# Kernel tuning notes

Measured on AMD Instinct MI355X. Metric: run time of the kernel, lower is better.

Reference implementation:

```python
import jax, jax.numpy as jnp
import numpy as np

EPS = 1e-5

def prelu(x, a):
    return jnp.where(x >= 0, x, a * x)

def batch_norm(x, axes):
    # training-mode BatchNorm with gamma=1, beta=0 (init values)
    m = jnp.mean(x, axis=axes, keepdims=True)
    v = jnp.var(x, axis=axes, keepdims=True)
    return (x - m) / jnp.sqrt(v + EPS)

def conv_branch(X, w, b):
    # X: [B,N,F]; Conv2d(1,1,(1,k)) over the feature axis, VALID
    lhs = X[:, None, :, :]                      # [B,1,N,F]
    rhs = w.reshape(1, 1, 1, -1)                # OIHW
    out = jax.lax.conv_general_dilated(lhs, rhs, (1, 1), 'VALID',
        dimension_numbers=('NCHW', 'OIHW', 'NCHW'))
    return out[:, 0] + b                        # [B,N,F-k+1]

def setup_inputs() -> dict:
    key = jax.random.key(0)
    ks = jax.random.split(key, 16)
    B, N, F, H, D = 8192, 29, 147, 4, 128
    d_cat = 429
    s = 0.05
    return {
        'X': jax.random.normal(ks[0], (B, N, F), jnp.float32),
        'corr': jax.random.uniform(ks[1], (B, N, N), jnp.float32),
        'w_c1': s * jax.random.normal(ks[2], (3,), jnp.float32),
        'b_c1': jnp.zeros((1,), jnp.float32),
        'w_c2': s * jax.random.normal(ks[3], (5,), jnp.float32),
        'b_c2': jnp.zeros((1,), jnp.float32),
        'w_c3': s * jax.random.normal(ks[4], (7,), jnp.float32),
        'b_c3': jnp.zeros((1,), jnp.float32),
        'a_cnn': 0.25 * jnp.ones((1,), jnp.float32),
        'Wg': s * jax.random.normal(ks[5], (d_cat, D), jnp.float32),
        'bg': jnp.zeros((D,), jnp.float32),
        'a_gnn': 0.25 * jnp.ones((1,), jnp.float32),
        'centroids': jax.random.normal(ks[6], (H, 1, D), jnp.float32),
        'head_w': s * jax.random.normal(ks[7], (H,), jnp.float32),
        'Wp': s * jax.random.normal(ks[8], (D, D), jnp.float32),
        'bp': jnp.zeros((D,), jnp.float32),
        'Wm1': s * jax.random.normal(ks[9], (D, D), jnp.float32),
        'bm1': jnp.zeros((D,), jnp.float32),
        'a_mlp': 0.25 * jnp.ones((1,), jnp.float32),
        'Wm2': s * jax.random.normal(ks[10], (D, 1), jnp.float32),
        'bm2': jnp.zeros((1,), jnp.float32),
    }

def reference(X, corr, w_c1, b_c1, w_c2, b_c2, w_c3, b_c3, a_cnn,
              Wg, bg, a_gnn, centroids, head_w, Wp, bp,
              Wm1, bm1, a_mlp, Wm2, bm2):
    # three conv branches + concat + PReLU + BN over node channels
    a1 = conv_branch(X, w_c1, b_c1)             # [B,29,145]
    a2 = conv_branch(X, w_c2, b_c2)             # [B,29,143]
    a3 = conv_branch(X, w_c3, b_c3)             # [B,29,141]
    x = prelu(jnp.concatenate([a1, a2, a3], axis=2), a_cnn)  # [B,29,429]
    x = batch_norm(x, (0, 2))
    # GraphConv: A x W + b
    x = jnp.einsum('bnm,bmd->bnd', corr, x) @ Wg + bg        # [B,29,128]
    x = prelu(x, a_gnn)
    x = batch_norm(x, (0, 2))
    # CoSimPool: multi-head cosine-sim attention assignment to 1 cluster
    xn = x / (jnp.linalg.norm(x, axis=-1, keepdims=True) + 1e-8)
    cn = centroids / (jnp.linalg.norm(centroids, axis=-1, keepdims=True) + 1e-8)
    sim = jnp.einsum('hmd,bnd->bhmn', cn, xn)                # [B,4,1,29]
    agg = jnp.einsum('h,bhmn->bmn', head_w, sim)             # 1x1 conv over heads
    C = jax.nn.softmax(agg, axis=-1)                         # [B,1,29]
    x = jnp.einsum('bmn,bnd->bmd', C, x) @ Wp + bp           # [B,1,128]
    x = x[:, 0]                                              # squeeze(1)
    x = batch_norm(x, (0,))
    h = prelu(x @ Wm1 + bm1, a_mlp)
    y = jax.nn.sigmoid(h @ Wm2 + bm2)                        # [B,1]
    return y
```

## Files before the change

### kernel.cpp

```cpp
#include <hip/hip_runtime.h>

#define B_    8192
#define N_    29
#define F_    147
#define DC    429
#define D_    128
#define ROWS  (B_*N_)
#define EPSBN 1e-5f

#define UTSTR   4096
#define RS_SH   3712

#define X3_OFF   16777216
#define ACC_OFF  (X3_OFF + B_*D_)
#define BN1_OFF  (ACC_OFF)
#define BN2_OFF  (ACC_OFF + 1856)
#define BN3_OFF  (ACC_OFF + 3712)
#define FIN_OFF  (ACC_OFF + 11904)
#define CSW_OFF  (FIN_OFF + 384)
#define V_OFF    (FIN_OFF + 512)
#define V1_OFF   (FIN_OFF + 640)
#define CSWP_OFF (FIN_OFF + 768)
#define IMG_OFF  (FIN_OFF + 1024)
#define WPI_OFF  (IMG_OFF + 28672)
#define WM1I_OFF (WPI_OFF + 8192)

typedef __bf16 bf16x8 __attribute__((ext_vector_type(8)));
typedef float  f32x4  __attribute__((ext_vector_type(4)));
typedef float  f32x2  __attribute__((ext_vector_type(2)));

__device__ __forceinline__ unsigned short f2bf(float f) {
  __bf16 h = (__bf16)f;
  return __builtin_bit_cast(unsigned short, h);
}
__device__ __forceinline__ float bf2f(unsigned u16) {
  return __uint_as_float(u16 << 16);
}
__device__ __forceinline__ unsigned packbf(f32x2 v) {
  return (unsigned)f2bf(v[0]) | ((unsigned)f2bf(v[1]) << 16);
}
__device__ __forceinline__ f32x2 pfma(f32x2 a, float s, f32x2 c) {
  return __builtin_elementwise_fma(a, (f32x2){s, s}, c);
}
__device__ __forceinline__ f32x2 prelu2(f32x2 v, float a) {
  f32x2 z = (f32x2){0.f, 0.f};
  return __builtin_elementwise_fma(__builtin_elementwise_min(v, z), (f32x2){a, a},
                                   __builtin_elementwise_max(v, z));
}
__device__ __forceinline__ void gload_lds4(const float* g, void* l) {
  __builtin_amdgcn_global_load_lds((const __attribute__((address_space(1))) void*)g,
                                   (__attribute__((address_space(3))) void*)l, 4, 0, 0);
}

#define TSTR 460
#define XROW 148
#define UTILS 34
#define ATSTR 136

__global__ void k0_setup(const float* __restrict__ Wg, const float* __restrict__ Wp,
                         const float* __restrict__ Wm1, const float* __restrict__ cent,
                         const float* __restrict__ hw, float* __restrict__ ws)
{
  const int tid = threadIdx.x;
  if (blockIdx.x < 16) {
    __shared__ float cs_l[8];
    const int kb = blockIdx.x * 8;
    if (tid < 8) cs_l[tid] = 0.f;
    __syncthreads();
    unsigned short* img = (unsigned short*)(ws + IMG_OFF);
    for (int i = tid; i < 8*448; i += 256) {
      int kk = i / 448, dk = i - kk*448;
      int k = kb + kk;
      int d;
      if      (dk < 145)  d = dk;
      else if (dk == 145) d = -1;
      else if (dk < 289)  d = dk - 1;
      else if (dk == 289) d = -1;
      else if (dk < 431)  d = dk - 2;
      else                d = -1;
      float v = (d >= 0) ? Wg[(size_t)d*D_ + k] : 0.f;
      img[(size_t)k*448 + dk] = f2bf(v);
      if (d >= 0) atomicAdd(&cs_l[kk], v);
    }
    __syncthreads();
    if (tid < 8) ws[CSW_OFF + kb + tid] = cs_l[tid];
  } else if (blockIdx.x == 16) {
    unsigned short* wpi = (unsigned short*)(ws + WPI_OFF);
    for (int i = tid; i < 16384; i += 256) {
      int k = i >> 7, c = i & 127;
      wpi[c*128 + k] = f2bf(Wp[k*128 + c]);
    }
    if (tid < 128) {
      float s = 0.f;
      for (int k = 0; k < 128; ++k) s += Wp[k*128 + tid];
      ws[CSWP_OFF + tid] = s;
    }
  } else if (blockIdx.x == 17) {
    unsigned short* wmi = (unsigned short*)(ws + WM1I_OFF);
    for (int i = tid; i < 16384; i += 256) {
      int k = i >> 7, c = i & 127;
      wmi[c*128 + k] = f2bf(Wm1[k*128 + c]);
    }
  } else {
    const int wv = tid >> 6, lane = tid & 63;
    if (wv == 0) {
      float vk0 = 0.f, vk1 = 0.f;
      for (int h = 0; h < 4; ++h) {
        float c0 = cent[h*D_ + lane];
        float c1 = cent[h*D_ + 64 + lane];
        float s = c0*c0 + c1*c1;
        #pragma unroll
        for (int off = 32; off >= 1; off >>= 1) s += __shfl_xor(s, off);
        float w = hw[h] / (sqrtf(s) + 1e-8f);
        vk0 = fmaf(c0, w, vk0);
        vk1 = fmaf(c1, w, vk1);
      }
      ws[V_OFF + lane]      = vk0;
      ws[V_OFF + 64 + lane] = vk1;
      float t = vk0 + vk1;
      #pragma unroll
      for (int off = 32; off >= 1; off >>= 1) t += __shfl_xor(t, off);
      if (lane == 0) ws[V1_OFF] = t;
    } else {
      for (int i = tid - 64; i < 11904; i += 192) ws[ACC_OFF + i] = 0.f;
    }
  }
}

__global__ __launch_bounds__(256, 5) void k1_conv_gemm(
    const float* __restrict__ X,
    const float* __restrict__ wc1, const float* __restrict__ bc1,
    const float* __restrict__ wc2, const float* __restrict__ bc2,
    const float* __restrict__ wc3, const float* __restrict__ bc3,
    const float* __restrict__ acnn, float* __restrict__ ws)
{
  __shared__ __align__(16) unsigned short t_s[32*TSTR];
  const int tid = threadIdx.x;
  const int b = blockIdx.x;
  const int wv = tid >> 6, lane = tid & 63;
  const int lrow = lane & 15, quad = lane >> 4;

  {
    const float* Xb = X + (size_t)b * (N_ * F_);
    unsigned* xd = (unsigned*)t_s;
    const int r0 = wv*8, r1 = (r0 + 8 < 29) ? r0 + 8 : 29;
    for (int r = r0; r < r1; ++r) {
      const float* src = Xb + r*147;
      unsigned* dst = xd + r*XROW;
      gload_lds4(src + lane, dst);
      gload_lds4(src + 64 + lane, dst + 64);
      if (lane < 19) gload_lds4(src + 128 + lane, dst + 128);
    }
    asm volatile("s_waitcnt vmcnt(0)" ::: "memory");
    __builtin_amdgcn_sched_barrier(0);
  }

  const float c10 = wc1[0], c11 = wc1[1], c12 = wc1[2], b1 = bc1[0];
  const float c20 = wc2[0], c21 = wc2[1], c22 = wc2[2], c23 = wc2[3], c24 = wc2[4], b2 = bc2[0];
  const float c30 = wc3[0], c31 = wc3[1], c32 = wc3[2], c33 = wc3[3], c34 = wc3[4],
              c35 = wc3[5], c36 = wc3[6], b3 = bc3[0];
  const float ap = acnn[0];

  const int nC = tid >> 3, qC = tid & 7;
  const bool act = (nC < 29);
  const int f0 = qC * 18;
  const int nld = act ? nC : 28;
  float xv[24];
  {
    const f32x2* xp = (const f32x2*)((const float*)t_s + nld*XROW + f0);
    #pragma unroll
    for (int j = 0; j < 12; ++j) {
      f32x2 t = xp[j];
      xv[2*j] = t[0]; xv[2*j+1] = t[1];
    }
  }
  __syncthreads();

  for (int i = tid; i < 3*448; i += 256) {
    int r = i / 448, c = i - r*448;
    t_s[(29 + r)*TSTR + c] = 0;
  }
  for (int i = tid; i < 29*19; i += 256) {
    int n = i / 19, j = i - n*19;
    int col = (j == 0) ? 145 : ((j == 1) ? 289 : (429 + j));
    t_s[n*TSTR + col] = 0;
  }

  {
    f32x2 s1v = (f32x2){0.f,0.f}, s2v = (f32x2){0.f,0.f};
    float s1t = 0.f, s2t = 0.f;
    unsigned short* tr = t_s + nC*TSTR + f0;
    if (act) {
      const int np2 = (qC < 7) ? 9 : 8;
      const int np3 = (qC < 7) ? 9 : 7;
      #pragma unroll
      for (int j = 0; j < 9; ++j) {
        const int k = 2*j;
        f32x2 xA = (f32x2){xv[k],   xv[k+1]};
        f32x2 xB = (f32x2){xv[k+1], xv[k+2]};
        f32x2 xC = (f32x2){xv[k+2], xv[k+3]};
        {
          f32x2 v1 = pfma(xA,c10, pfma(xB,c11, pfma(xC,c12, (f32x2){b1,b1})));
          v1 = prelu2(v1, ap);
          s1v += v1; s2v = __builtin_elementwise_fma(v1, v1, s2v);
          *(unsigned*)(tr + k) = packbf(v1);
        }
        if (j < np2) {
          f32x2 xD = (f32x2){xv[k+3], xv[k+4]};
          f32x2 xE = (f32x2){xv[k+4], xv[k+5]};
          f32x2 v2 = pfma(xA,c20, pfma(xB,c21, pfma(xC,c22, pfma(xD,c23, pfma(xE,c24, (f32x2){b2,b2})))));
          v2 = prelu2(v2, ap);
          s1v += v2; s2v = __builtin_elementwise_fma(v2, v2, s2v);
          *(unsigned*)(tr + 146 + k) = packbf(v2);
        }
        if (j < np3) {
          f32x2 xD = (f32x2){xv[k+3], xv[k+4]};
          f32x2 xE = (f32x2){xv[k+4], xv[k+5]};
          f32x2 xF = (f32x2){xv[k+5], xv[k+6]};
          f32x2 xG = (f32x2){xv[k+6], xv[k+7]};
          f32x2 v3 = pfma(xA,c30, pfma(xB,c31, pfma(xC,c32, pfma(xD,c33, pfma(xE,c34, pfma(xF,c35, pfma(xG,c36, (f32x2){b3,b3})))))));
          v3 = prelu2(v3, ap);
          s1v += v3; s2v = __builtin_elementwise_fma(v3, v3, s2v);
          *(unsigned*)(tr + 290 + k) = packbf(v3);
        }
      }
      if (qC == 7) {
        float u1 = fmaf(xv[18],c10, fmaf(xv[19],c11, fmaf(xv[20],c12, b1)));
        u1 = (u1 >= 0.f) ? u1 : ap*u1;
        s1t += u1; s2t = fmaf(u1, u1, s2t);
        tr[18] = f2bf(u1);
        float u2 = fmaf(xv[16],c20, fmaf(xv[17],c21, fmaf(xv[18],c22, fmaf(xv[19],c23, fmaf(xv[20],c24, b2)))));
        u2 = (u2 >= 0.f) ? u2 : ap*u2;
        s1t += u2; s2t = fmaf(u2, u2, s2t);
        tr[146 + 16] = f2bf(u2);
        float u3 = fmaf(xv[14],c30, fmaf(xv[15],c31, fmaf(xv[16],c32, fmaf(xv[17],c33, fmaf(xv[18],c34, fmaf(xv[19],c35, fmaf(xv[20],c36, b3)))))));
        u3 = (u3 >= 0.f) ? u3 : ap*u3;
        s1t += u3; s2t = fmaf(u3, u3, s2t);
        tr[290 + 14] = f2bf(u3);
      }
    }
    float s1 = s1v[0] + s1v[1] + s1t;
    float s2 = s2v[0] + s2v[1] + s2t;
    #pragma unroll
    for (int off = 4; off >= 1; off >>= 1) {
      s1 += __shfl_xor(s1, off);
      s2 += __shfl_xor(s2, off);
    }
    if (act && qC == 0) {
      float* bn1 = ws + BN1_OFF + (size_t)(blockIdx.x & 31) * 58;
      atomicAdd(&bn1[nC*2+0], s1);
      atomicAdd(&bn1[nC*2+1], s2);
    }
  }
  __syncthreads();

  const int n0 = wv * 32;
  const unsigned short* imgp = (const unsigned short*)(ws + IMG_OFF);
  const unsigned short* gB0 = imgp + (size_t)(n0 + lrow)*448 + quad*8;
  const unsigned short* gB1 = gB0 + 16*448;
  const unsigned short* tA = t_s + quad*8;

  f32x4 a00 = (f32x4){0.f,0.f,0.f,0.f}, a01 = a00, a10 = a00, a11 = a00;
  bf16x8 Br0[4], Br1[4];
  #pragma unroll
  for (int j = 0; j < 4; ++j) {
    Br0[j] = *(const bf16x8*)(gB0 + j*32);
    Br1[j] = *(const bf16x8*)(gB1 + j*32);
  }
  #pragma unroll
  for (int ks = 0; ks < 14; ++ks) {
    bf16x8 Bc0 = Br0[ks & 3], Bc1 = Br1[ks & 3];
    if (ks < 10) {
      Br0[ks & 3] = *(const bf16x8*)(gB0 + (ks+4)*32);
      Br1[ks & 3] = *(const bf16x8*)(gB1 + (ks+4)*32);
    }
    bf16x8 A0 = *(const bf16x8*)(tA + lrow*TSTR + ks*32);
    bf16x8 A1 = *(const bf16x8*)(tA + (16+lrow)*TSTR + ks*32);
    a00 = __builtin_amdgcn_mfma_f32_16x16x32_bf16(A0, Bc0, a00, 0, 0, 0);
    a01 = __builtin_amdgcn_mfma_f32_16x16x32_bf16(A0, Bc1, a01, 0, 0, 0);
    a10 = __builtin_amdgcn_mfma_f32_16x16x32_bf16(A1, Bc0, a10, 0, 0, 0);
    a11 = __builtin_amdgcn_mfma_f32_16x16x32_bf16(A1, Bc1, a11, 0, 0, 0);
  }
  __syncthreads();

  {
    unsigned* ut32 = (unsigned*)t_s;
    const int fb0 = n0 + lrow, fb1 = n0 + 16 + lrow;
    #pragma unroll
    for (int jp = 0; jp < 2; ++jp) {
      int w = quad*2 + jp;
      ut32[fb0*17 + w]     = packbf((f32x2){a00[2*jp], a00[2*jp+1]});
      ut32[fb1*17 + w]     = packbf((f32x2){a01[2*jp], a01[2*jp+1]});
      ut32[fb0*17 + 8 + w] = packbf((f32x2){a10[2*jp], a10[2*jp+1]});
      ut32[fb1*17 + 8 + w] = packbf((f32x2){a11[2*jp], a11[2*jp+1]});
    }
  }
  __syncthreads();
  {
    const unsigned* u32t = (const unsigned*)t_s;
    unsigned short* ws16 = (unsigned short*)ws;
    unsigned* Ug = (unsigned*)(ws16 + (size_t)b * UTSTR);
    #pragma unroll
    for (int it = 0; it < 8; ++it) {
      int idx = tid + it*256;
      int f = idx >> 4, pr = idx & 15;
      Ug[f*16 + pr] = u32t[f*17 + pr];
    }
  }
}

__global__ void k2_bn1f(float* __restrict__ ws)
{
  const int n = threadIdx.x;
  if (n < 29) {
    float s1 = 0.f, s2 = 0.f;
    #pragma unroll 4
    for (int s = 0; s < 32; ++s) {
      s1 += ws[BN1_OFF + s*58 + n*2 + 0];
      s2 += ws[BN1_OFF + s*58 + n*2 + 1];
    }
    const float inv = 1.f / (float)(B_ * DC);
    float mean = s1 * inv;
    float var  = s2 * inv - mean * mean;
    ws[FIN_OFF + n]      = mean;
    ws[FIN_OFF + 32 + n] = rsqrtf(var + EPSBN);
  }
}

__global__ __launch_bounds__(256) void k3_gnn(
    const float* __restrict__ corr, const float* __restrict__ bg,
    const float* __restrict__ agnn, float* __restrict__ ws)
{
  __shared__ float cwf[841];
  __shared__ unsigned short a_s[32*40];
  __shared__ float m1s[29], is1s[29], cms[32];
  __shared__ float sts0[4][32], sts1[4][32], sts2[4][32];

  const int b = blockIdx.x, tid = threadIdx.x;
  const int wv = tid >> 6, lane = tid & 63;
  const int lrow = lane & 15, quad = lane >> 4;
  unsigned short* Utb = (unsigned short*)ws + (size_t)b * UTSTR;

  const int f0 = wv * 32;
  bf16x8 B0 = *(const bf16x8*)&Utb[(f0      + lrow)*32 + quad*8];
  bf16x8 B1 = *(const bf16x8*)&Utb[(f0 + 16 + lrow)*32 + quad*8];

  if (tid < 29) {
    m1s[tid]  = ws[FIN_OFF + tid];
    is1s[tid] = ws[FIN_OFF + 32 + tid];
  }
  const float* cb = corr + (size_t)b * 841;
  for (int i = tid; i < 841; i += 256) cwf[i] = cb[i];
  __syncthreads();

  {
    float pp[4];
    #pragma unroll
    for (int it = 0; it < 4; ++it) {
      int i = tid + it*256;
      int n = i >> 5, m = i & 31;
      bool val = (n < 29 && m < 29);
      float v = val ? cwf[n*29 + m] * is1s[m] : 0.f;
      a_s[n*40 + m] = f2bf(v);
      pp[it] = val ? v * m1s[m] : 0.f;
    }
    #pragma unroll
    for (int off = 16; off >= 1; off >>= 1) {
      #pragma unroll
      for (int it = 0; it < 4; ++it) pp[it] += __shfl_xor(pp[it], off);
    }
    #pragma unroll
    for (int it = 0; it < 4; ++it) {
      int i = tid + it*256;
      if ((i & 31) == 0 && (i >> 5) < 29) cms[i >> 5] = pp[it];
    }
  }
  __syncthreads();

  bf16x8 A0 = *(const bf16x8*)&a_s[lrow*40 + quad*8];
  bf16x8 A1 = *(const bf16x8*)&a_s[(16 + lrow)*40 + quad*8];
  f32x4 acc[2][2];
  acc[0][0] = (f32x4){0.f,0.f,0.f,0.f}; acc[0][1] = (f32x4){0.f,0.f,0.f,0.f};
  acc[1][0] = (f32x4){0.f,0.f,0.f,0.f}; acc[1][1] = (f32x4){0.f,0.f,0.f,0.f};
  acc[0][0] = __builtin_amdgcn_mfma_f32_16x16x32_bf16(A0, B0, acc[0][0], 0, 0, 0);
  acc[0][1] = __builtin_amdgcn_mfma_f32_16x16x32_bf16(A0, B1, acc[0][1], 0, 0, 0);
  acc[1][0] = __builtin_amdgcn_mfma_f32_16x16x32_bf16(A1, B0, acc[1][0], 0, 0, 0);
  acc[1][1] = __builtin_amdgcn_mfma_f32_16x16x32_bf16(A1, B1, acc[1][1], 0, 0, 0);
  __syncthreads();

  const float ag = agnn[0];
  const float vA  = ws[V_OFF  + f0 + lrow],      vB  = ws[V_OFF  + f0 + 16 + lrow];
  const float csA = ws[CSW_OFF + f0 + lrow],     csB = ws[CSW_OFF + f0 + 16 + lrow];
  const float bgA = bg[f0 + lrow],               bgB = bg[f0 + 16 + lrow];

  float psy[8], psy2[8], psv[8];
  #pragma unroll
  for (int mt = 0; mt < 2; ++mt) {
    #pragma unroll
    for (int i = 0; i < 4; ++i) {
      int idx = mt*4 + i;
      int n = mt*16 + quad*4 + i;
      float y0 = acc[mt][0][i] - cms[n & 31]*csA + bgA;
      float y1 = acc[mt][1][i] - cms[n & 31]*csB + bgB;
      y0 = (y0 >= 0.f) ? y0 : ag*y0;
      y1 = (y1 >= 0.f) ? y1 : ag*y1;
      if (n < 29) {
        Utb[n*D_ + f0 + lrow]      = f2bf(y0);
        Utb[n*D_ + f0 + 16 + lrow] = f2bf(y1);
      }
      psy[idx]  = y0 + y1;
      psy2[idx] = fmaf(y0, y0, y1*y1);
      psv[idx]  = fmaf(y0, vA, y1*vB);
    }
  }
  #pragma unroll
  for (int off = 8; off >= 1; off >>= 1) {
    #pragma unroll
    for (int idx = 0; idx < 8; ++idx) {
      psy[idx]  += __shfl_xor(psy[idx],  off);
      psy2[idx] += __shfl_xor(psy2[idx], off);
      psv[idx]  += __shfl_xor(psv[idx],  off);
    }
  }
  if (lrow == 0) {
    #pragma unroll
    for (int mt = 0; mt < 2; ++mt) {
      #pragma unroll
      for (int i = 0; i < 4; ++i) {
        int idx = mt*4 + i;
        int n = mt*16 + quad*4 + i;
        if (n < 29) {
          sts0[wv][n] = psy[idx];
          sts1[wv][n] = psy2[idx];
          sts2[wv][n] = psv[idx];
        }
      }
    }
  }
  __syncthreads();
  if (tid < 29) {
    float S1 = sts0[0][tid] + sts0[1][tid] + sts0[2][tid] + sts0[3][tid];
    float S2 = sts1[0][tid] + sts1[1][tid] + sts1[2][tid] + sts1[3][tid];
    float Sv = sts2[0][tid] + sts2[1][tid] + sts2[2][tid] + sts2[3][tid];
    float* rs = (float*)(Utb + RS_SH);
    rs[tid]      = S1;
    rs[29 + tid] = S2;
    rs[58 + tid] = Sv;
    float* bn2 = ws + BN2_OFF + (size_t)(b & 31) * 58;
    atomicAdd(&bn2[tid*2+0], S1);
    atomicAdd(&bn2[tid*2+1], S2);
  }
}

__global__ __launch_bounds__(256) void k4_pool(
    const float* __restrict__ bpv, float* __restrict__ ws)
{
  __shared__ unsigned short Atile[32*ATSTR];
  __shared__ float m2s[29], is2s[29], koffs[32];
  const int tid = threadIdx.x, wv = tid >> 6, lane = tid & 63;
  const int b0 = blockIdx.x * 32;
  const unsigned short* U16 = (const unsigned short*)ws;

  if (tid < 29) {
    float s1 = 0.f, s2 = 0.f;
    #pragma unroll 4
    for (int s = 0; s < 32; ++s) {
      s1 += ws[BN2_OFF + s*58 + tid*2 + 0];
      s2 += ws[BN2_OFF + s*58 + tid*2 + 1];
    }
    const float inv = 1.f / (float)(B_ * D_);
    float mean = s1 * inv, var = s2 * inv - mean * mean;
    m2s[tid] = mean; is2s[tid] = rsqrtf(var + EPSBN);
  }
  __syncthreads();

  const float V1 = ws[V1_OFF];
  unsigned* At32 = (unsigned*)Atile;
  for (int mb = 0; mb < 8; ++mb) {
    const int m = wv*8 + mb;
    const unsigned short* yb = U16 + (size_t)(b0 + m) * UTSTR;
    const float* rs = (const float*)(yb + RS_SH);
    float agg = -1e30f, m2 = 0.f, is2 = 0.f;
    if (lane < 29) {
      float S1 = rs[lane], S2 = rs[29+lane], Sv = rs[58+lane];
      m2 = m2s[lane]; is2 = is2s[lane];
      float ss = fmaxf(S2 - 2.f*m2*S1 + 128.f*m2*m2, 0.f);
      agg = (is2*(Sv - m2*V1)) / (is2*sqrtf(ss) + 1e-8f);
    }
    float mx = agg;
    #pragma unroll
    for (int off = 32; off >= 1; off >>= 1) mx = fmaxf(mx, __shfl_xor(mx, off));
    float e = (lane < 29) ? __expf(agg - mx) : 0.f;
    float den = e, kof = e*is2*m2;
    #pragma unroll
    for (int off = 32; off >= 1; off >>= 1) { den += __shfl_xor(den, off); kof += __shfl_xor(kof, off); }
    float rden = 1.f / den;
    float c = e * is2 * rden;
    if (lane == 0) koffs[m] = kof * rden;
    const unsigned* y32 = (const unsigned*)yb;
    float p0 = 0.f, p1 = 0.f;
    #pragma unroll
    for (int n = 0; n < 29; ++n) {
      float cn = __shfl(c, n);
      unsigned u = y32[n*64 + lane];
      p0 = fmaf(cn, bf2f(u & 0xffffu), p0);
      p1 = fmaf(cn, bf2f(u >> 16), p1);
    }
    At32[m*68 + lane] = (unsigned)f2bf(p0) | ((unsigned)f2bf(p1) << 16);
  }
  __syncthreads();

  const int lrow = lane & 15, quad = lane >> 4;
  const int n0 = wv * 32;
  const unsigned short* wpi = (const unsigned short*)(ws + WPI_OFF);
  f32x4 acc[2][2];
  acc[0][0] = (f32x4){0.f,0.f,0.f,0.f}; acc[0][1] = acc[0][0];
  acc[1][0] = acc[0][0]; acc[1][1] = acc[0][0];
  #pragma unroll
  for (int ks = 0; ks < 4; ++ks) {
    bf16x8 A0 = *(const bf16x8*)&Atile[lrow*ATSTR + ks*32 + quad*8];
    bf16x8 A1 = *(const bf16x8*)&Atile[(16+lrow)*ATSTR + ks*32 + quad*8];
    bf16x8 Bq0 = *(const bf16x8*)&wpi[(size_t)(n0 + lrow)*128 + ks*32 + quad*8];
    bf16x8 Bq1 = *(const bf16x8*)&wpi[(size_t)(n0 + 16 + lrow)*128 + ks*32 + quad*8];
    acc[0][0] = __builtin_amdgcn_mfma_f32_16x16x32_bf16(A0, Bq0, acc[0][0], 0, 0, 0);
    acc[0][1] = __builtin_amdgcn_mfma_f32_16x16x32_bf16(A0, Bq1, acc[0][1], 0, 0, 0);
    acc[1][0] = __builtin_amdgcn_mfma_f32_16x16x32_bf16(A1, Bq0, acc[1][0], 0, 0, 0);
    acc[1][1] = __builtin_amdgcn_mfma_f32_16x16x32_bf16(A1, Bq1, acc[1][1], 0, 0, 0);
  }

  float* bn3 = ws + BN3_OFF + (size_t)(blockIdx.x & 31) * 256;
  #pragma unroll
  for (int nt = 0; nt < 2; ++nt) {
    int col = n0 + nt*16 + lrow;
    float cswp = ws[CSWP_OFF + col], bp = bpv[col];
    float s1c = 0.f, s2c = 0.f;
    #pragma unroll
    for (int mt = 0; mt < 2; ++mt) {
      #pragma unroll
      for (int i = 0; i < 4; ++i) {
        int m = mt*16 + quad*4 + i;
        float x3 = acc[mt][nt][i] - koffs[m]*cswp + bp;
        ws[X3_OFF + (size_t)(b0 + m)*D_ + col] = x3;
        s1c += x3; s2c = fmaf(x3, x3, s2c);
      }
    }
    s1c += __shfl_xor(s1c, 16); s1c += __shfl_xor(s1c, 32);
    s2c += __shfl_xor(s2c, 16); s2c += __shfl_xor(s2c, 32);
    if (quad == 0) {
      atomicAdd(&bn3[col*2+0], s1c);
      atomicAdd(&bn3[col*2+1], s2c);
    }
  }
}

__global__ __launch_bounds__(256) void k5_mlp(
    const float* __restrict__ bm1, const float* __restrict__ amlp,
    const float* __restrict__ Wm2, const float* __restrict__ bm2,
    float* __restrict__ ws, float* __restrict__ out)
{
  __shared__ unsigned short Atile[32*ATSTR];
  __shared__ float m3s[128], is3s[128], logit_s[32];
  const int tid = threadIdx.x, wv = tid >> 6, lane = tid & 63;
  const int b0 = blockIdx.x * 32;

  if (tid < 128) {
    float s1 = 0.f, s2 = 0.f;
    #pragma unroll 4
    for (int s = 0; s < 32; ++s) {
      s1 += ws[BN3_OFF + s*256 + tid*2 + 0];
      s2 += ws[BN3_OFF + s*256 + tid*2 + 1];
    }
    const float inv = 1.f / (float)B_;
    float mean = s1 * inv, var = s2 * inv - mean * mean;
    m3s[tid] = mean; is3s[tid] = rsqrtf(var + EPSBN);
  }
  if (tid >= 128 && tid < 160) logit_s[tid-128] = 0.f;
  __syncthreads();

  for (int it = 0; it < 16; ++it) {
    int idx = tid + it*256;
    int row = idx >> 7, col = idx & 127;
    float v = (ws[X3_OFF + (size_t)(b0+row)*D_ + col] - m3s[col]) * is3s[col];
    Atile[row*ATSTR + col] = f2bf(v);
  }
  __syncthreads();

  const int lrow = lane & 15, quad = lane >> 4;
  const int n0 = wv * 32;
  const unsigned short* wmi = (const unsigned short*)(ws + WM1I_OFF);
  f32x4 acc[2][2];
  acc[0][0] = (f32x4){0.f,0.f,0.f,0.f}; acc[0][1] = acc[0][0];
  acc[1][0] = acc[0][0]; acc[1][1] = acc[0][0];
  #pragma unroll
  for (int ks = 0; ks < 4; ++ks) {
    bf16x8 A0 = *(const bf16x8*)&Atile[lrow*ATSTR + ks*32 + quad*8];
    bf16x8 A1 = *(const bf16x8*)&Atile[(16+lrow)*ATSTR + ks*32 + quad*8];
    bf16x8 Bq0 = *(const bf16x8*)&wmi[(size_t)(n0 + lrow)*128 + ks*32 + quad*8];
    bf16x8 Bq1 = *(const bf16x8*)&wmi[(size_t)(n0 + 16 + lrow)*128 + ks*32 + quad*8];
    acc[0][0] = __builtin_amdgcn_mfma_f32_16x16x32_bf16(A0, Bq0, acc[0][0], 0, 0, 0);
    acc[0][1] = __builtin_amdgcn_mfma_f32_16x16x32_bf16(A0, Bq1, acc[0][1], 0, 0, 0);
    acc[1][0] = __builtin_amdgcn_mfma_f32_16x16x32_bf16(A1, Bq0, acc[1][0], 0, 0, 0);
    acc[1][1] = __builtin_amdgcn_mfma_f32_16x16x32_bf16(A1, Bq1, acc[1][1], 0, 0, 0);
  }

  const float am = amlp[0];
  float bmc[2], wm2c[2];
  #pragma unroll
  for (int nt = 0; nt < 2; ++nt) {
    int col = n0 + nt*16 + lrow;
    bmc[nt] = bm1[col]; wm2c[nt] = Wm2[col];
  }
  #pragma unroll
  for (int mt = 0; mt < 2; ++mt) {
    #pragma unroll
    for (int i = 0; i < 4; ++i) {
      float pm = 0.f;
      #pragma unroll
      for (int nt = 0; nt < 2; ++nt) {
        float h = acc[mt][nt][i] + bmc[nt];
        h = (h >= 0.f) ? h : am*h;
        pm = fmaf(h, wm2c[nt], pm);
      }
      #pragma unroll
      for (int off = 8; off >= 1; off >>= 1) pm += __shfl_xor(pm, off);
      if (lrow == 0) atomicAdd(&logit_s[mt*16 + quad*4 + i], pm);
    }
  }
  __syncthreads();
  if (tid < 32) {
    float logit = logit_s[tid] + bm2[0];
    out[b0 + tid] = 1.f / (1.f + expf(-logit));
  }
}

extern "C" void kernel_launch(void* const* d_in, const int* in_sizes, int n_in,
                              void* d_out, int out_size, void* d_ws, size_t ws_size,
                              hipStream_t stream)
{
  (void)in_sizes; (void)n_in; (void)out_size; (void)ws_size;
  const float* X    = (const float*)d_in[0];
  const float* corr = (const float*)d_in[1];
  const float* wc1  = (const float*)d_in[2];
  const float* bc1  = (const float*)d_in[3];
  const float* wc2  = (const float*)d_in[4];
  const float* bc2  = (const float*)d_in[5];
  const float* wc3  = (const float*)d_in[6];
  const float* bc3  = (const float*)d_in[7];
  const float* acnn = (const float*)d_in[8];
  const float* Wg   = (const float*)d_in[9];
  const float* bg   = (const float*)d_in[10];
  const float* agnn = (const float*)d_in[11];
  const float* cent = (const float*)d_in[12];
  const float* hw   = (const float*)d_in[13];
  const float* Wp   = (const float*)d_in[14];
  const float* bp   = (const float*)d_in[15];
  const float* Wm1  = (const float*)d_in[16];
  const float* bm1  = (const float*)d_in[17];
  const float* amlp = (const float*)d_in[18];
  const float* Wm2  = (const float*)d_in[19];
  const float* bm2  = (const float*)d_in[20];
  float* ws  = (float*)d_ws;
  float* out = (float*)d_out;

  k0_setup<<<19, 256, 0, stream>>>(Wg, Wp, Wm1, cent, hw, ws);
  k1_conv_gemm<<<B_, 256, 0, stream>>>(X, wc1, bc1, wc2, bc2, wc3, bc3, acnn, ws);
  k2_bn1f<<<1, 64, 0, stream>>>(ws);
  k3_gnn<<<B_, 256, 0, stream>>>(corr, bg, agnn, ws);
  k4_pool<<<B_/32, 256, 0, stream>>>(bp, ws);
  k5_mlp<<<B_/32, 256, 0, stream>>>(bm1, amlp, Wm2, bm2, ws, out);
}
```

Baseline: 453.9 us.

## Process four batch items per block in conv-GEMM with register prefetch of X

The conv+GEMM kernel now loops over four batch items per block. It prefetches the next item's X slice into registers while computing the current one, replacing the per-block async global-to-LDS copy. Padding-zeroing is hoisted out of the loop, and the output transpose gets its own LDS buffer. The B-operand register prefetch depth is halved and the occupancy hint lowered, trading occupancy and load coalescing for amortized setup and overlap.

```diff
diff --git a/kernel.cpp b/kernel.cpp
--- a/kernel.cpp
+++ b/kernel.cpp
@@ -47,15 +47,11 @@
   return __builtin_elementwise_fma(__builtin_elementwise_min(v, z), (f32x2){a, a},
                                    __builtin_elementwise_max(v, z));
 }
-__device__ __forceinline__ void gload_lds4(const float* g, void* l) {
-  __builtin_amdgcn_global_load_lds((const __attribute__((address_space(1))) void*)g,
-                                   (__attribute__((address_space(3))) void*)l, 4, 0, 0);
-}
 
 #define TSTR 460
-#define XROW 148
 #define UTILS 34
 #define ATSTR 136
+#define NB_IT 4
 
 __global__ void k0_setup(const float* __restrict__ Wg, const float* __restrict__ Wp,
                          const float* __restrict__ Wm1, const float* __restrict__ cent,
@@ -127,7 +123,7 @@
   }
 }
 
-__global__ __launch_bounds__(256, 5) void k1_conv_gemm(
+__global__ __launch_bounds__(256, 4) void k1_conv_gemm(
     const float* __restrict__ X,
     const float* __restrict__ wc1, const float* __restrict__ bc1,
     const float* __restrict__ wc2, const float* __restrict__ bc2,
@@ -135,24 +131,25 @@
     const float* __restrict__ acnn, float* __restrict__ ws)
 {
   __shared__ __align__(16) unsigned short t_s[32*TSTR];
+  __shared__ __align__(16) unsigned tp_s[2176];
   const int tid = threadIdx.x;
-  const int b = blockIdx.x;
   const int wv = tid >> 6, lane = tid & 63;
   const int lrow = lane & 15, quad = lane >> 4;
-
-  {
-    const float* Xb = X + (size_t)b * (N_ * F_);
-    unsigned* xd = (unsigned*)t_s;
-    const int r0 = wv*8, r1 = (r0 + 8 < 29) ? r0 + 8 : 29;
-    for (int r = r0; r < r1; ++r) {
-      const float* src = Xb + r*147;
-      unsigned* dst = xd + r*XROW;
-      gload_lds4(src + lane, dst);
-      gload_lds4(src + 64 + lane, dst + 64);
-      if (lane < 19) gload_lds4(src + 128 + lane, dst + 128);
-    }
-    asm volatile("s_waitcnt vmcnt(0)" ::: "memory");
-    __builtin_amdgcn_sched_barrier(0);
+  const int b0 = blockIdx.x * NB_IT;
+
+  const int nC = tid >> 3, qC = tid & 7;
+  const bool act = (nC < 29);
+  const int f0 = qC * 18;
+  const int nld = act ? nC : 28;
+
+  for (int i = tid; i < 3*448; i += 256) {
+    int r = i / 448, c = i - r*448;
+    t_s[(29 + r)*TSTR + c] = 0;
+  }
+  for (int i = tid; i < 29*19; i += 256) {
+    int n = i / 19, j = i - n*19;
+    int col = (j == 0) ? 145 : ((j == 1) ? 289 : (429 + j));
+    t_s[n*TSTR + col] = 0;
   }
 
   const float c10 = wc1[0], c11 = wc1[1], c12 = wc1[2], b1 = bc1[0];
@@ -161,150 +158,149 @@
               c35 = wc3[5], c36 = wc3[6], b3 = bc3[0];
   const float ap = acnn[0];
 
-  const int nC = tid >> 3, qC = tid & 7;
-  const bool act = (nC < 29);
-  const int f0 = qC * 18;
-  const int nld = act ? nC : 28;
-  float xv[24];
-  {
-    const f32x2* xp = (const f32x2*)((const float*)t_s + nld*XROW + f0);
-    #pragma unroll
-    for (int j = 0; j < 12; ++j) {
-      f32x2 t = xp[j];
-      xv[2*j] = t[0]; xv[2*j+1] = t[1];
-    }
-  }
-  __syncthreads();
-
-  for (int i = tid; i < 3*448; i += 256) {
-    int r = i / 448, c = i - r*448;
-    t_s[(29 + r)*TSTR + c] = 0;
-  }
-  for (int i = tid; i < 29*19; i += 256) {
-    int n = i / 19, j = i - n*19;
-    int col = (j == 0) ? 145 : ((j == 1) ? 289 : (429 + j));
-    t_s[n*TSTR + col] = 0;
-  }
-
-  {
-    f32x2 s1v = (f32x2){0.f,0.f}, s2v = (f32x2){0.f,0.f};
-    float s1t = 0.f, s2t = 0.f;
-    unsigned short* tr = t_s + nC*TSTR + f0;
-    if (act) {
-      const int np2 = (qC < 7) ? 9 : 8;
-      const int np3 = (qC < 7) ? 9 : 7;
-      #pragma unroll
-      for (int j = 0; j < 9; ++j) {
-        const int k = 2*j;
-        f32x2 xA = (f32x2){xv[k],   xv[k+1]};
-        f32x2 xB = (f32x2){xv[k+1], xv[k+2]};
-        f32x2 xC = (f32x2){xv[k+2], xv[k+3]};
-        {
-          f32x2 v1 = pfma(xA,c10, pfma(xB,c11, pfma(xC,c12, (f32x2){b1,b1})));
-          v1 = prelu2(v1, ap);
-          s1v += v1; s2v = __builtin_elementwise_fma(v1, v1, s2v);
-          *(unsigned*)(tr + k) = packbf(v1);
-        }
-        if (j < np2) {
-          f32x2 xD = (f32x2){xv[k+3], xv[k+4]};
-          f32x2 xE = (f32x2){xv[k+4], xv[k+5]};
-          f32x2 v2 = pfma(xA,c20, pfma(xB,c21, pfma(xC,c22, pfma(xD,c23, pfma(xE,c24, (f32x2){b2,b2})))));
-          v2 = prelu2(v2, ap);
-          s1v += v2; s2v = __builtin_elementwise_fma(v2, v2, s2v);
-          *(unsigned*)(tr + 146 + k) = packbf(v2);
-        }
-        if (j < np3) {
-          f32x2 xD = (f32x2){xv[k+3], xv[k+4]};
-          f32x2 xE = (f32x2){xv[k+4], xv[k+5]};
-          f32x2 xF = (f32x2){xv[k+5], xv[k+6]};
-          f32x2 xG = (f32x2){xv[k+6], xv[k+7]};
-          f32x2 v3 = pfma(xA,c30, pfma(xB,c31, pfma(xC,c32, pfma(xD,c33, pfma(xE,c34, pfma(xF,c35, pfma(xG,c36, (f32x2){b3,b3})))))));
-          v3 = prelu2(v3, ap);
-          s1v += v3; s2v = __builtin_elementwise_fma(v3, v3, s2v);
-          *(unsigned*)(tr + 290 + k) = packbf(v3);
-        }
-      }
-      if (qC == 7) {
-        float u1 = fmaf(xv[18],c10, fmaf(xv[19],c11, fmaf(xv[20],c12, b1)));
-        u1 = (u1 >= 0.f) ? u1 : ap*u1;
-        s1t += u1; s2t = fmaf(u1, u1, s2t);
-        tr[18] = f2bf(u1);
-        float u2 = fmaf(xv[16],c20, fmaf(xv[17],c21, fmaf(xv[18],c22, fmaf(xv[19],c23, fmaf(xv[20],c24, b2)))));
-        u2 = (u2 >= 0.f) ? u2 : ap*u2;
-        s1t += u2; s2t = fmaf(u2, u2, s2t);
-        tr[146 + 16] = f2bf(u2);
-        float u3 = fmaf(xv[14],c30, fmaf(xv[15],c31, fmaf(xv[16],c32, fmaf(xv[17],c33, fmaf(xv[18],c34, fmaf(xv[19],c35, fmaf(xv[20],c36, b3)))))));
-        u3 = (u3 >= 0.f) ? u3 : ap*u3;
-        s1t += u3; s2t = fmaf(u3, u3, s2t);
-        tr[290 + 14] = f2bf(u3);
-      }
-    }
-    float s1 = s1v[0] + s1v[1] + s1t;
-    float s2 = s2v[0] + s2v[1] + s2t;
-    #pragma unroll
-    for (int off = 4; off >= 1; off >>= 1) {
-      s1 += __shfl_xor(s1, off);
-      s2 += __shfl_xor(s2, off);
-    }
-    if (act && qC == 0) {
-      float* bn1 = ws + BN1_OFF + (size_t)(blockIdx.x & 31) * 58;
-      atomicAdd(&bn1[nC*2+0], s1);
-      atomicAdd(&bn1[nC*2+1], s2);
-    }
-  }
-  __syncthreads();
-
   const int n0 = wv * 32;
   const unsigned short* imgp = (const unsigned short*)(ws + IMG_OFF);
   const unsigned short* gB0 = imgp + (size_t)(n0 + lrow)*448 + quad*8;
   const unsigned short* gB1 = gB0 + 16*448;
   const unsigned short* tA = t_s + quad*8;
 
-  f32x4 a00 = (f32x4){0.f,0.f,0.f,0.f}, a01 = a00, a10 = a00, a11 = a00;
-  bf16x8 Br0[4], Br1[4];
-  #pragma unroll
-  for (int j = 0; j < 4; ++j) {
-    Br0[j] = *(const bf16x8*)(gB0 + j*32);
-    Br1[j] = *(const bf16x8*)(gB1 + j*32);
-  }
-  #pragma unroll
-  for (int ks = 0; ks < 14; ++ks) {
-    bf16x8 Bc0 = Br0[ks & 3], Bc1 = Br1[ks & 3];
-    if (ks < 10) {
-      Br0[ks & 3] = *(const bf16x8*)(gB0 + (ks+4)*32);
-      Br1[ks & 3] = *(const bf16x8*)(gB1 + (ks+4)*32);
-    }
-    bf16x8 A0 = *(const bf16x8*)(tA + lrow*TSTR + ks*32);
-    bf16x8 A1 = *(const bf16x8*)(tA + (16+lrow)*TSTR + ks*32);
-    a00 = __builtin_amdgcn_mfma_f32_16x16x32_bf16(A0, Bc0, a00, 0, 0, 0);
-    a01 = __builtin_amdgcn_mfma_f32_16x16x32_bf16(A0, Bc1, a01, 0, 0, 0);
-    a10 = __builtin_amdgcn_mfma_f32_16x16x32_bf16(A1, Bc0, a10, 0, 0, 0);
-    a11 = __builtin_amdgcn_mfma_f32_16x16x32_bf16(A1, Bc1, a11, 0, 0, 0);
-  }
-  __syncthreads();
-
+  float xv[24];
   {
-    unsigned* ut32 = (unsigned*)t_s;
-    const int fb0 = n0 + lrow, fb1 = n0 + 16 + lrow;
-    #pragma unroll
-    for (int jp = 0; jp < 2; ++jp) {
-      int w = quad*2 + jp;
-      ut32[fb0*17 + w]     = packbf((f32x2){a00[2*jp], a00[2*jp+1]});
-      ut32[fb1*17 + w]     = packbf((f32x2){a01[2*jp], a01[2*jp+1]});
-      ut32[fb0*17 + 8 + w] = packbf((f32x2){a10[2*jp], a10[2*jp+1]});
-      ut32[fb1*17 + 8 + w] = packbf((f32x2){a11[2*jp], a11[2*jp+1]});
-    }
-  }
-  __syncthreads();
-  {
-    const unsigned* u32t = (const unsigned*)t_s;
-    unsigned short* ws16 = (unsigned short*)ws;
-    unsigned* Ug = (unsigned*)(ws16 + (size_t)b * UTSTR);
-    #pragma unroll
-    for (int it = 0; it < 8; ++it) {
-      int idx = tid + it*256;
-      int f = idx >> 4, pr = idx & 15;
-      Ug[f*16 + pr] = u32t[f*17 + pr];
+    const float* xr = X + (size_t)b0*(N_*F_) + nld*F_ + f0;
+    #pragma unroll
+    for (int j = 0; j < 24; ++j) xv[j] = xr[j];
+  }
+
+  #pragma unroll
+  for (int it = 0; it < NB_IT; ++it) {
+    const int b = b0 + it;
+
+    float xn[24];
+    if (it + 1 < NB_IT) {
+      const float* xr = X + (size_t)(b+1)*(N_*F_) + nld*F_ + f0;
+      #pragma unroll
+      for (int j = 0; j < 24; ++j) xn[j] = xr[j];
+    }
+
+    {
+      f32x2 s1v = (f32x2){0.f,0.f}, s2v = (f32x2){0.f,0.f};
+      float s1t = 0.f, s2t = 0.f;
+      unsigned short* tr = t_s + nC*TSTR + f0;
+      if (act) {
+        const int np2 = (qC < 7) ? 9 : 8;
+        const int np3 = (qC < 7) ? 9 : 7;
+        #pragma unroll
+        for (int j = 0; j < 9; ++j) {
+          const int k = 2*j;
+          f32x2 xA = (f32x2){xv[k],   xv[k+1]};
+          f32x2 xB = (f32x2){xv[k+1], xv[k+2]};
+          f32x2 xC = (f32x2){xv[k+2], xv[k+3]};
+          {
+            f32x2 v1 = pfma(xA,c10, pfma(xB,c11, pfma(xC,c12, (f32x2){b1,b1})));
+            v1 = prelu2(v1, ap);
+            s1v += v1; s2v = __builtin_elementwise_fma(v1, v1, s2v);
+            *(unsigned*)(tr + k) = packbf(v1);
+          }
+          if (j < np2) {
+            f32x2 xD = (f32x2){xv[k+3], xv[k+4]};
+            f32x2 xE = (f32x2){xv[k+4], xv[k+5]};
+            f32x2 v2 = pfma(xA,c20, pfma(xB,c21, pfma(xC,c22, pfma(xD,c23, pfma(xE,c24, (f32x2){b2,b2})))));
+            v2 = prelu2(v2, ap);
+            s1v += v2; s2v = __builtin_elementwise_fma(v2, v2, s2v);
+            *(unsigned*)(tr + 146 + k) = packbf(v2);
+          }
+          if (j < np3) {
+            f32x2 xD = (f32x2){xv[k+3], xv[k+4]};
+            f32x2 xE = (f32x2){xv[k+4], xv[k+5]};
+            f32x2 xF = (f32x2){xv[k+5], xv[k+6]};
+            f32x2 xG = (f32x2){xv[k+6], xv[k+7]};
+            f32x2 v3 = pfma(xA,c30, pfma(xB,c31, pfma(xC,c32, pfma(xD,c33, pfma(xE,c34, pfma(xF,c35, pfma(xG,c36, (f32x2){b3,b3})))))));
+            v3 = prelu2(v3, ap);
+            s1v += v3; s2v = __builtin_elementwise_fma(v3, v3, s2v);
+            *(unsigned*)(tr + 290 + k) = packbf(v3);
+          }
+        }
+        if (qC == 7) {
+          float u1 = fmaf(xv[18],c10, fmaf(xv[19],c11, fmaf(xv[20],c12, b1)));
+          u1 = (u1 >= 0.f) ? u1 : ap*u1;
+          s1t += u1; s2t = fmaf(u1, u1, s2t);
+          tr[18] = f2bf(u1);
+          float u2 = fmaf(xv[16],c20, fmaf(xv[17],c21, fmaf(xv[18],c22, fmaf(xv[19],c23, fmaf(xv[20],c24, b2)))));
+          u2 = (u2 >= 0.f) ? u2 : ap*u2;
+          s1t += u2; s2t = fmaf(u2, u2, s2t);
+          tr[146 + 16] = f2bf(u2);
+          float u3 = fmaf(xv[14],c30, fmaf(xv[15],c31, fmaf(xv[16],c32, fmaf(xv[17],c33, fmaf(xv[18],c34, fmaf(xv[19],c35, fmaf(xv[20],c36, b3)))))));
+          u3 = (u3 >= 0.f) ? u3 : ap*u3;
+          s1t += u3; s2t = fmaf(u3, u3, s2t);
+          tr[290 + 14] = f2bf(u3);
+        }
+      }
+      float s1 = s1v[0] + s1v[1] + s1t;
+      float s2 = s2v[0] + s2v[1] + s2t;
+      #pragma unroll
+      for (int off = 4; off >= 1; off >>= 1) {
+        s1 += __shfl_xor(s1, off);
+        s2 += __shfl_xor(s2, off);
+      }
+      if (act && qC == 0) {
+        float* bn1 = ws + BN1_OFF + (size_t)(blockIdx.x & 31) * 58;
+        atomicAdd(&bn1[nC*2+0], s1);
+        atomicAdd(&bn1[nC*2+1], s2);
+      }
+    }
+    __syncthreads();
+
+    f32x4 a00 = (f32x4){0.f,0.f,0.f,0.f}, a01 = a00, a10 = a00, a11 = a00;
+    {
+      bf16x8 Br0[2], Br1[2];
+      Br0[0] = *(const bf16x8*)(gB0);
+      Br1[0] = *(const bf16x8*)(gB1);
+      Br0[1] = *(const bf16x8*)(gB0 + 32);
+      Br1[1] = *(const bf16x8*)(gB1 + 32);
+      #pragma unroll
+      for (int ks = 0; ks < 14; ++ks) {
+        bf16x8 Bc0 = Br0[ks & 1], Bc1 = Br1[ks & 1];
+        if (ks < 12) {
+          Br0[ks & 1] = *(const bf16x8*)(gB0 + (ks+2)*32);
+          Br1[ks & 1] = *(const bf16x8*)(gB1 + (ks+2)*32);
+        }
+        bf16x8 A0 = *(const bf16x8*)(tA + lrow*TSTR + ks*32);
+        bf16x8 A1 = *(const bf16x8*)(tA + (16+lrow)*TSTR + ks*32);
+        a00 = __builtin_amdgcn_mfma_f32_16x16x32_bf16(A0, Bc0, a00, 0, 0, 0);
+        a01 = __builtin_amdgcn_mfma_f32_16x16x32_bf16(A0, Bc1, a01, 0, 0, 0);
+        a10 = __builtin_amdgcn_mfma_f32_16x16x32_bf16(A1, Bc0, a10, 0, 0, 0);
+        a11 = __builtin_amdgcn_mfma_f32_16x16x32_bf16(A1, Bc1, a11, 0, 0, 0);
+      }
+    }
+    __syncthreads();
+
+    {
+      const int fb0 = n0 + lrow, fb1 = n0 + 16 + lrow;
+      #pragma unroll
+      for (int jp = 0; jp < 2; ++jp) {
+        int w = quad*2 + jp;
+        tp_s[fb0*17 + w]     = packbf((f32x2){a00[2*jp], a00[2*jp+1]});
+        tp_s[fb1*17 + w]     = packbf((f32x2){a01[2*jp], a01[2*jp+1]});
+        tp_s[fb0*17 + 8 + w] = packbf((f32x2){a10[2*jp], a10[2*jp+1]});
+        tp_s[fb1*17 + 8 + w] = packbf((f32x2){a11[2*jp], a11[2*jp+1]});
+      }
+    }
+    __syncthreads();
+
+    {
+      unsigned short* ws16 = (unsigned short*)ws;
+      unsigned* Ug = (unsigned*)(ws16 + (size_t)b * UTSTR);
+      #pragma unroll
+      for (int itc = 0; itc < 8; ++itc) {
+        int idx = tid + itc*256;
+        int f = idx >> 4, pr = idx & 15;
+        Ug[f*16 + pr] = tp_s[f*17 + pr];
+      }
+    }
+
+    if (it + 1 < NB_IT) {
+      #pragma unroll
+      for (int j = 0; j < 24; ++j) xv[j] = xn[j];
     }
   }
 }
@@ -663,7 +659,7 @@
   float* out = (float*)d_out;
 
   k0_setup<<<19, 256, 0, stream>>>(Wg, Wp, Wm1, cent, hw, ws);
-  k1_conv_gemm<<<B_, 256, 0, stream>>>(X, wc1, bc1, wc2, bc2, wc3, bc3, acnn, ws);
+  k1_conv_gemm<<<B_/NB_IT, 256, 0, stream>>>(X, wc1, bc1, wc2, bc2, wc3, bc3, acnn, ws);
   k2_bn1f<<<1, 64, 0, stream>>>(ws);
   k3_gnn<<<B_, 256, 0, stream>>>(corr, bg, agnn, ws);
   k4_pool<<<B_/32, 256, 0, stream>>>(bp, ws);
```

Result: no change. 462.5 us (+1.9%).
